# Optimization experiments

Hardware: AMD Instinct MI355X
Metric: run time of the kernel (lower is better)

Reference implementation:

```python
import jax, jax.numpy as jnp
import numpy as np

N_NODES = 50000
N_EDGES = 800000
F_IN, H, C1, C2 = 256, 128, 4, 3


def gcn_conv(x, W, b, src, dst, n_nodes):
    # PyG GCNConv: add self-loops, symmetric normalization D^-1/2 A D^-1/2,
    # linear transform, scatter-add aggregation at dst, then bias.
    loop = jnp.arange(n_nodes, dtype=src.dtype)
    s = jnp.concatenate([src, loop])
    d = jnp.concatenate([dst, loop])
    deg = jax.ops.segment_sum(jnp.ones_like(d, dtype=x.dtype), d, num_segments=n_nodes)
    dinv = jnp.where(deg > 0, jax.lax.rsqrt(deg), 0.0)
    norm = dinv[s] * dinv[d]                      # [E+N]
    h = x @ W                                     # [N, out]
    msg = h[s] * norm[:, None]                    # gather + scale
    out = jax.ops.segment_sum(msg, d, num_segments=n_nodes)  # scatter-add
    return out + b


def setup_inputs() -> dict:
    key = jax.random.key(0)
    ks = jax.random.split(key, 10)
    x = jax.random.normal(ks[0], (N_NODES, F_IN), dtype=jnp.float32)
    edge_index = jax.random.randint(ks[1], (2, N_EDGES), 0, N_NODES, dtype=jnp.int32)
    def lin(k, fan_in, fan_out):
        bound = 1.0 / np.sqrt(fan_in)
        kw, kb = jax.random.split(k)
        W = jax.random.uniform(kw, (fan_in, fan_out), jnp.float32, -bound, bound)
        b = jax.random.uniform(kb, (fan_out,), jnp.float32, -bound, bound)
        return W, b
    W1, b1 = lin(ks[2], F_IN, H)
    W2, b2 = lin(ks[3], H, H)
    Wh1, bh1 = lin(ks[4], H, C1)
    Wh2, bh2 = lin(ks[5], H, C2)
    return {"x": x, "edge_index": edge_index, "W1": W1, "b1": b1,
            "W2": W2, "b2": b2, "Wh1": Wh1, "bh1": bh1, "Wh2": Wh2, "bh2": bh2}


def reference(x, edge_index, W1, b1, W2, b2, Wh1, bh1, Wh2, bh2):
    # Eval-mode forward (dropout p=0.5 is identity at inference; l2_classifier=False).
    src, dst = edge_index[0], edge_index[1]
    h = gcn_conv(x, W1, b1, src, dst, N_NODES)
    h = jax.nn.relu(h)
    h = gcn_conv(h, W2, b2, src, dst, N_NODES)
    out1 = h @ Wh1 + bh1
    out2 = h @ Wh2 + bh2
    return (out1, out2, h)
```

## Files before the change

### kernel.cpp

```cpp
#include <hip/hip_runtime.h>

#define NN 50000
#define NE 800000
#define FIN 256
#define HD 128
#define CAP 96

typedef unsigned int uint;
typedef unsigned short ushort;
typedef __attribute__((ext_vector_type(8))) short short8v;
typedef __attribute__((ext_vector_type(4))) float f32x4;

__device__ inline ushort f2bf(float f) {
    uint u = __float_as_uint(f);
    u += 0x7fffu + ((u >> 16) & 1u);
    return (ushort)(u >> 16);
}
__device__ inline float bf2f(ushort h) { return __uint_as_float(((uint)h) << 16); }
__device__ inline void unpack2(uint u, float& a, float& b) {
    a = __uint_as_float(u << 16);
    b = __uint_as_float(u & 0xffff0000u);
}


__global__ void build_buckets(const int* __restrict__ ei, int* __restrict__ cnt,
                              int* __restrict__ bucket) {
    int e = blockIdx.x * 256 + threadIdx.x;
    if (e >= NE) return;
    int s = ei[e];
    int d = ei[NE + e];
    int pos = atomicAdd(&cnt[d], 1);
    if (pos < CAP) bucket[d * CAP + pos] = s;
}

__global__ void compute_dinv(const int* __restrict__ cnt, float* __restrict__ dinv) {
    int v = blockIdx.x * 256 + threadIdx.x;
    if (v < NN) dinv[v] = rsqrtf((float)cnt[v] + 1.0f);
}


template<int K>
__global__ void prep_wt(const float* __restrict__ W, ushort* __restrict__ Wt) {
    int idx = blockIdx.x * 256 + threadIdx.x;
    if (idx >= K * 128) return;
    int k = idx >> 7, col = idx & 127;
    Wt[col * K + k] = f2bf(W[idx]);
}


template<int K>
__global__ __launch_bounds__(256) void gemm_mfma(const float* __restrict__ A,
                                                 const ushort* __restrict__ Wt,
                                                 const float* __restrict__ dscale,
                                                 ushort* __restrict__ C, int M) {
    __shared__ ushort Ah[64][40];
    __shared__ ushort Al[64][40];
    __shared__ ushort Bt[128][40];
    const int tid  = threadIdx.x;
    const int wid  = tid >> 6;
    const int lane = tid & 63;
    const int fr   = lane & 15;
    const int kg   = lane >> 4;

    const int blockRow = blockIdx.x * 64;

    f32x4 acc[8];
#pragma unroll
    for (int n = 0; n < 8; ++n) acc[n] = (f32x4){0.f, 0.f, 0.f, 0.f};

    const int s_ar = tid >> 3;
    const int s_ak = (tid & 7) << 2;

    for (int k0 = 0; k0 < K; k0 += 32) {
#pragma unroll
        for (int i = 0; i < 2; ++i) {
            int r = i * 32 + s_ar;
            int row = blockRow + r;
            float4 av = make_float4(0.f, 0.f, 0.f, 0.f);
            if (row < M) av = *(const float4*)(A + (size_t)row * K + k0 + s_ak);
            ushort h0 = f2bf(av.x), h1 = f2bf(av.y), h2 = f2bf(av.z), h3 = f2bf(av.w);
            ushort l0 = f2bf(av.x - bf2f(h0)), l1 = f2bf(av.y - bf2f(h1));
            ushort l2 = f2bf(av.z - bf2f(h2)), l3 = f2bf(av.w - bf2f(h3));
            uint2 hw, lw;
            hw.x = (uint)h0 | ((uint)h1 << 16); hw.y = (uint)h2 | ((uint)h3 << 16);
            lw.x = (uint)l0 | ((uint)l1 << 16); lw.y = (uint)l2 | ((uint)l3 << 16);
            *(uint2*)&Ah[r][s_ak] = hw;
            *(uint2*)&Al[r][s_ak] = lw;
        }
#pragma unroll
        for (int i = 0; i < 2; ++i) {
            int id = i * 256 + tid;
            int col = id >> 2;
            int kc = (id & 3) << 3;
            *(uint4*)&Bt[col][kc] = *(const uint4*)(Wt + (size_t)col * K + k0 + kc);
        }
        __syncthreads();
        short8v a_h = *(short8v*)&Ah[(wid << 4) + fr][kg << 3];
        short8v a_l = *(short8v*)&Al[(wid << 4) + fr][kg << 3];
#pragma unroll
        for (int n = 0; n < 8; ++n) {
            short8v b = *(short8v*)&Bt[(n << 4) + fr][kg << 3];
            acc[n] = __builtin_amdgcn_mfma_f32_16x16x32_bf16(a_h, b, acc[n], 0, 0, 0);
            acc[n] = __builtin_amdgcn_mfma_f32_16x16x32_bf16(a_l, b, acc[n], 0, 0, 0);
        }
        __syncthreads();
    }

    const int rbase = blockRow + (wid << 4) + (kg << 2);
#pragma unroll
    for (int r = 0; r < 4; ++r) {
        int row = rbase + r;
        if (row < M) {
            float ds = dscale[row];
#pragma unroll
            for (int n = 0; n < 8; ++n)
                C[(size_t)row * 128 + (n << 4) + fr] = f2bf(ds * acc[n][r]);
        }
    }
}


template<int RELU, int HEADS>
__global__ __launch_bounds__(256) void aggregate(const ushort* __restrict__ hb,
                                                 const int* __restrict__ cnt,
                                                 const int* __restrict__ bucket,
                                                 const float* __restrict__ dinv,
                                                 const float* __restrict__ bias,
                                                 float* __restrict__ out,
                                                 const float* __restrict__ Wh1,
                                                 const float* __restrict__ bh1,
                                                 const float* __restrict__ Wh2,
                                                 const float* __restrict__ bh2,
                                                 float* __restrict__ out1,
                                                 float* __restrict__ out2) {
    int v = (blockIdx.x << 2) + (threadIdx.x >> 6);
    if (v >= NN) return;
    const int lane = threadIdx.x & 63;
    const int g = lane >> 4;
    const int q = lane & 15;
    int c = cnt[v]; if (c > CAP) c = CAP;
    const int total = c + 1;
    const float di = dinv[v];
    const int* bk = bucket + (size_t)v * CAP;

    float acc[8];
#pragma unroll
    for (int j = 0; j < 8; ++j) acc[j] = 0.f;

    auto slotof = [&](int k) -> int {
        return k < c ? bk[k] : (k == c ? v : NN);
    };
    auto rowload = [&](int s) -> uint4 {
        return *(const uint4*)(hb + (size_t)s * 128 + (q << 3));
    };

    int sA = slotof(g);
    int sB = slotof(4 + g);
    uint4 rA = rowload(sA);
    uint4 rB = rowload(sB);
    int sC = slotof(8 + g);
    int sD = slotof(12 + g);

    for (int e = 0; e < total; e += 8) {
        uint4 rA2 = rowload(sC);
        uint4 rB2 = rowload(sD);
        sC = slotof(e + 16 + g);
        sD = slotof(e + 20 + g);
        float f0, f1, f2, f3, f4, f5, f6, f7;
        unpack2(rA.x, f0, f1); unpack2(rA.y, f2, f3);
        unpack2(rA.z, f4, f5); unpack2(rA.w, f6, f7);
        acc[0] += f0; acc[1] += f1; acc[2] += f2; acc[3] += f3;
        acc[4] += f4; acc[5] += f5; acc[6] += f6; acc[7] += f7;
        unpack2(rB.x, f0, f1); unpack2(rB.y, f2, f3);
        unpack2(rB.z, f4, f5); unpack2(rB.w, f6, f7);
        acc[0] += f0; acc[1] += f1; acc[2] += f2; acc[3] += f3;
        acc[4] += f4; acc[5] += f5; acc[6] += f6; acc[7] += f7;
        rA = rA2; rB = rB2;
    }

#pragma unroll
    for (int j = 0; j < 8; ++j) {
        acc[j] += __shfl_xor(acc[j], 16);
        acc[j] += __shfl_xor(acc[j], 32);
    }

    float4 bb0 = *(const float4*)(bias + (q << 3));
    float4 bb1 = *(const float4*)(bias + (q << 3) + 4);
    float o[8];
    o[0] = fmaf(di, acc[0], bb0.x); o[1] = fmaf(di, acc[1], bb0.y);
    o[2] = fmaf(di, acc[2], bb0.z); o[3] = fmaf(di, acc[3], bb0.w);
    o[4] = fmaf(di, acc[4], bb1.x); o[5] = fmaf(di, acc[5], bb1.y);
    o[6] = fmaf(di, acc[6], bb1.z); o[7] = fmaf(di, acc[7], bb1.w);
    if (RELU) {
#pragma unroll
        for (int j = 0; j < 8; ++j) o[j] = fmaxf(o[j], 0.f);
    }

    if (g < 2) {
        int j0 = (g & 1) << 2;
        *(float4*)(out + (size_t)v * 128 + (q << 3) + j0) =
            make_float4(o[j0], o[j0 + 1], o[j0 + 2], o[j0 + 3]);
    }

    if (HEADS) {
        const int kb = q << 3;
        float p[7];
#pragma unroll
        for (int cc = 0; cc < 4; ++cc) {
            float s = 0.f;
#pragma unroll
            for (int j = 0; j < 8; ++j) s = fmaf(o[j], Wh1[(kb + j) * 4 + cc], s);
            p[cc] = s;
        }
#pragma unroll
        for (int cc = 0; cc < 3; ++cc) {
            float s = 0.f;
#pragma unroll
            for (int j = 0; j < 8; ++j) s = fmaf(o[j], Wh2[(kb + j) * 3 + cc], s);
            p[4 + cc] = s;
        }
#pragma unroll
        for (int i = 0; i < 7; ++i) {
            float s = p[i];
            s += __shfl_xor(s, 1);
            s += __shfl_xor(s, 2);
            s += __shfl_xor(s, 4);
            s += __shfl_xor(s, 8);
            p[i] = s;
        }
        if (lane == 0) {
            out1[(size_t)v * 4 + 0] = p[0] + bh1[0];
            out1[(size_t)v * 4 + 1] = p[1] + bh1[1];
            out1[(size_t)v * 4 + 2] = p[2] + bh1[2];
            out1[(size_t)v * 4 + 3] = p[3] + bh1[3];
            out2[(size_t)v * 3 + 0] = p[4] + bh2[0];
            out2[(size_t)v * 3 + 1] = p[5] + bh2[1];
            out2[(size_t)v * 3 + 2] = p[6] + bh2[2];
        }
    }
}


extern "C" void kernel_launch(void* const* d_in, const int* in_sizes, int n_in,
                              void* d_out, int out_size, void* d_ws, size_t ws_size,
                              hipStream_t stream) {
    const float* x   = (const float*)d_in[0];
    const int*   ei  = (const int*)d_in[1];
    const float* W1  = (const float*)d_in[2];
    const float* b1  = (const float*)d_in[3];
    const float* W2  = (const float*)d_in[4];
    const float* b2  = (const float*)d_in[5];
    const float* Wh1 = (const float*)d_in[6];
    const float* bh1 = (const float*)d_in[7];
    const float* Wh2 = (const float*)d_in[8];
    const float* bh2 = (const float*)d_in[9];

    float* out1 = (float*)d_out;
    float* out2 = out1 + (size_t)NN * 4;
    float* hout = out2 + (size_t)NN * 3;

    char* ws = (char*)d_ws;
    auto alloc = [&](size_t bytes) { char* p = ws; ws += (bytes + 255) & ~(size_t)255; return p; };
    int*    cnt    = (int*)   alloc((size_t)NN * 4);
    float*  dinv   = (float*) alloc((size_t)NN * 4);
    int*    bucket = (int*)   alloc((size_t)NN * CAP * 4);
    ushort* hlinb  = (ushort*)alloc((size_t)(NN + 1) * HD * 2);
    float*  hagg   = (float*) alloc((size_t)NN * HD * 4);
    ushort* Wt1    = (ushort*)alloc((size_t)128 * FIN * 2);
    ushort* Wt2    = (ushort*)alloc((size_t)128 * HD * 2);

    hipMemsetAsync(cnt, 0, (size_t)NN * 4, stream);
    hipMemsetAsync(hlinb + (size_t)NN * HD, 0, HD * 2, stream);
    build_buckets<<<(NE + 255) / 256, 256, 0, stream>>>(ei, cnt, bucket);
    compute_dinv<<<(NN + 255) / 256, 256, 0, stream>>>(cnt, dinv);
    prep_wt<FIN><<<(FIN * 128 + 255) / 256, 256, 0, stream>>>(W1, Wt1);
    prep_wt<HD><<<(HD * 128 + 255) / 256, 256, 0, stream>>>(W2, Wt2);

    gemm_mfma<FIN><<<(NN + 63) / 64, 256, 0, stream>>>(x, Wt1, dinv, hlinb, NN);
    aggregate<1, 0><<<(NN + 3) / 4, 256, 0, stream>>>(hlinb, cnt, bucket, dinv, b1, hagg,
                                                      nullptr, nullptr, nullptr, nullptr,
                                                      nullptr, nullptr);

    gemm_mfma<HD><<<(NN + 63) / 64, 256, 0, stream>>>(hagg, Wt2, dinv, hlinb, NN);
    aggregate<0, 1><<<(NN + 3) / 4, 256, 0, stream>>>(hlinb, cnt, bucket, dinv, b2, hout,
                                                      Wh1, bh1, Wh2, bh2, out1, out2);
}
```

Before: 298.2 us.

## Process four nodes per wavefront with a continuous chunk stream in aggregation

```diff
diff --git a/kernel.cpp b/kernel.cpp
--- a/kernel.cpp
+++ b/kernel.cpp
@@ -133,110 +133,130 @@
                                                  const float* __restrict__ bh2,
                                                  float* __restrict__ out1,
                                                  float* __restrict__ out2) {
-    int v = (blockIdx.x << 2) + (threadIdx.x >> 6);
-    if (v >= NN) return;
+    const int wv = blockIdx.x * 4 + (threadIdx.x >> 6);
+    const int v0 = wv << 2;
+    if (v0 >= NN) return;
     const int lane = threadIdx.x & 63;
     const int g = lane >> 4;
     const int q = lane & 15;
-    int c = cnt[v]; if (c > CAP) c = CAP;
-    const int total = c + 1;
-    const float di = dinv[v];
-    const int* bk = bucket + (size_t)v * CAP;
-
-    float acc[8];
-#pragma unroll
-    for (int j = 0; j < 8; ++j) acc[j] = 0.f;
-
-    auto slotof = [&](int k) -> int {
-        return k < c ? bk[k] : (k == c ? v : NN);
+
+    const int c0 = min(cnt[v0], CAP),     c1 = min(cnt[v0 + 1], CAP),
+              c2 = min(cnt[v0 + 2], CAP), c3 = min(cnt[v0 + 3], CAP);
+    const float di0 = dinv[v0],     di1 = dinv[v0 + 1],
+                di2 = dinv[v0 + 2], di3 = dinv[v0 + 3];
+    const int tb1 = (c0 + 4) >> 2;
+    const int tb2 = tb1 + ((c1 + 4) >> 2);
+    const int tb3 = tb2 + ((c2 + 4) >> 2);
+    const int nch = tb3 + ((c3 + 4) >> 2);
+
+    auto slot_index = [&](int t) -> int {
+        if (t >= nch) return NN;
+        int nd = (t >= tb1) + (t >= tb2) + (t >= tb3);
+        int tb = nd == 0 ? 0  : nd == 1 ? tb1 : nd == 2 ? tb2 : tb3;
+        int c  = nd == 0 ? c0 : nd == 1 ? c1  : nd == 2 ? c2  : c3;
+        int idx = ((t - tb) << 2) + g;
+        int vv = v0 + nd;
+        return idx < c ? bucket[(size_t)vv * CAP + idx] : (idx == c ? vv : NN);
     };
     auto rowload = [&](int s) -> uint4 {
         return *(const uint4*)(hb + (size_t)s * 128 + (q << 3));
     };
 
-    int sA = slotof(g);
-    int sB = slotof(4 + g);
-    uint4 rA = rowload(sA);
-    uint4 rB = rowload(sB);
-    int sC = slotof(8 + g);
-    int sD = slotof(12 + g);
-
-    for (int e = 0; e < total; e += 8) {
-        uint4 rA2 = rowload(sC);
-        uint4 rB2 = rowload(sD);
-        sC = slotof(e + 16 + g);
-        sD = slotof(e + 20 + g);
+    float acc[8];
+#pragma unroll
+    for (int j = 0; j < 8; ++j) acc[j] = 0.f;
+
+    auto consume = [&](uint4 r) {
         float f0, f1, f2, f3, f4, f5, f6, f7;
-        unpack2(rA.x, f0, f1); unpack2(rA.y, f2, f3);
-        unpack2(rA.z, f4, f5); unpack2(rA.w, f6, f7);
+        unpack2(r.x, f0, f1); unpack2(r.y, f2, f3);
+        unpack2(r.z, f4, f5); unpack2(r.w, f6, f7);
         acc[0] += f0; acc[1] += f1; acc[2] += f2; acc[3] += f3;
         acc[4] += f4; acc[5] += f5; acc[6] += f6; acc[7] += f7;
-        unpack2(rB.x, f0, f1); unpack2(rB.y, f2, f3);
-        unpack2(rB.z, f4, f5); unpack2(rB.w, f6, f7);
-        acc[0] += f0; acc[1] += f1; acc[2] += f2; acc[3] += f3;
-        acc[4] += f4; acc[5] += f5; acc[6] += f6; acc[7] += f7;
-        rA = rA2; rB = rB2;
-    }
-
-#pragma unroll
-    for (int j = 0; j < 8; ++j) {
-        acc[j] += __shfl_xor(acc[j], 16);
-        acc[j] += __shfl_xor(acc[j], 32);
-    }
-
-    float4 bb0 = *(const float4*)(bias + (q << 3));
-    float4 bb1 = *(const float4*)(bias + (q << 3) + 4);
-    float o[8];
-    o[0] = fmaf(di, acc[0], bb0.x); o[1] = fmaf(di, acc[1], bb0.y);
-    o[2] = fmaf(di, acc[2], bb0.z); o[3] = fmaf(di, acc[3], bb0.w);
-    o[4] = fmaf(di, acc[4], bb1.x); o[5] = fmaf(di, acc[5], bb1.y);
-    o[6] = fmaf(di, acc[6], bb1.z); o[7] = fmaf(di, acc[7], bb1.w);
-    if (RELU) {
-#pragma unroll
-        for (int j = 0; j < 8; ++j) o[j] = fmaxf(o[j], 0.f);
-    }
-
-    if (g < 2) {
-        int j0 = (g & 1) << 2;
-        *(float4*)(out + (size_t)v * 128 + (q << 3) + j0) =
-            make_float4(o[j0], o[j0 + 1], o[j0 + 2], o[j0 + 3]);
-    }
-
-    if (HEADS) {
-        const int kb = q << 3;
-        float p[7];
-#pragma unroll
-        for (int cc = 0; cc < 4; ++cc) {
-            float s = 0.f;
-#pragma unroll
-            for (int j = 0; j < 8; ++j) s = fmaf(o[j], Wh1[(kb + j) * 4 + cc], s);
-            p[cc] = s;
-        }
-#pragma unroll
-        for (int cc = 0; cc < 3; ++cc) {
-            float s = 0.f;
-#pragma unroll
-            for (int j = 0; j < 8; ++j) s = fmaf(o[j], Wh2[(kb + j) * 3 + cc], s);
-            p[4 + cc] = s;
-        }
-#pragma unroll
-        for (int i = 0; i < 7; ++i) {
-            float s = p[i];
-            s += __shfl_xor(s, 1);
-            s += __shfl_xor(s, 2);
-            s += __shfl_xor(s, 4);
-            s += __shfl_xor(s, 8);
-            p[i] = s;
-        }
-        if (lane == 0) {
-            out1[(size_t)v * 4 + 0] = p[0] + bh1[0];
-            out1[(size_t)v * 4 + 1] = p[1] + bh1[1];
-            out1[(size_t)v * 4 + 2] = p[2] + bh1[2];
-            out1[(size_t)v * 4 + 3] = p[3] + bh1[3];
-            out2[(size_t)v * 3 + 0] = p[4] + bh2[0];
-            out2[(size_t)v * 3 + 1] = p[5] + bh2[1];
-            out2[(size_t)v * 3 + 2] = p[6] + bh2[2];
-        }
+    };
+
+    auto flush = [&](int nd) {
+        float o[8];
+#pragma unroll
+        for (int j = 0; j < 8; ++j) {
+            float t = acc[j];
+            t += __shfl_xor(t, 16);
+            t += __shfl_xor(t, 32);
+            o[j] = t;
+            acc[j] = 0.f;
+        }
+        const float di = nd == 0 ? di0 : nd == 1 ? di1 : nd == 2 ? di2 : di3;
+        const int v = v0 + nd;
+        float4 bb0 = *(const float4*)(bias + (q << 3));
+        float4 bb1 = *(const float4*)(bias + (q << 3) + 4);
+        o[0] = fmaf(di, o[0], bb0.x); o[1] = fmaf(di, o[1], bb0.y);
+        o[2] = fmaf(di, o[2], bb0.z); o[3] = fmaf(di, o[3], bb0.w);
+        o[4] = fmaf(di, o[4], bb1.x); o[5] = fmaf(di, o[5], bb1.y);
+        o[6] = fmaf(di, o[6], bb1.z); o[7] = fmaf(di, o[7], bb1.w);
+        if (RELU) {
+#pragma unroll
+            for (int j = 0; j < 8; ++j) o[j] = fmaxf(o[j], 0.f);
+        }
+        if (g < 2) {
+            int j0 = (g & 1) << 2;
+            *(float4*)(out + (size_t)v * 128 + (q << 3) + j0) =
+                make_float4(o[j0], o[j0 + 1], o[j0 + 2], o[j0 + 3]);
+        }
+        if (HEADS) {
+            const int kb = q << 3;
+            float p[7];
+#pragma unroll
+            for (int cc = 0; cc < 4; ++cc) {
+                float s = 0.f;
+#pragma unroll
+                for (int j = 0; j < 8; ++j) s = fmaf(o[j], Wh1[(kb + j) * 4 + cc], s);
+                p[cc] = s;
+            }
+#pragma unroll
+            for (int cc = 0; cc < 3; ++cc) {
+                float s = 0.f;
+#pragma unroll
+                for (int j = 0; j < 8; ++j) s = fmaf(o[j], Wh2[(kb + j) * 3 + cc], s);
+                p[4 + cc] = s;
+            }
+#pragma unroll
+            for (int i = 0; i < 7; ++i) {
+                float s = p[i];
+                s += __shfl_xor(s, 1);
+                s += __shfl_xor(s, 2);
+                s += __shfl_xor(s, 4);
+                s += __shfl_xor(s, 8);
+                p[i] = s;
+            }
+            if (lane == 0) {
+                out1[(size_t)v * 4 + 0] = p[0] + bh1[0];
+                out1[(size_t)v * 4 + 1] = p[1] + bh1[1];
+                out1[(size_t)v * 4 + 2] = p[2] + bh1[2];
+                out1[(size_t)v * 4 + 3] = p[3] + bh1[3];
+                out2[(size_t)v * 3 + 0] = p[4] + bh2[0];
+                out2[(size_t)v * 3 + 1] = p[5] + bh2[1];
+                out2[(size_t)v * 3 + 2] = p[6] + bh2[2];
+            }
+        }
+    };
+
+    int sP2 = slot_index(2);
+    int sP3 = slot_index(3);
+    uint4 rA = rowload(slot_index(0));
+    uint4 rB = rowload(slot_index(1));
+
+    int nd = 0;
+    int flushT = tb1 - 1;
+    for (int t = 0; t < nch; ++t) {
+        uint4 rN = rowload(sP2);
+        sP2 = sP3;
+        sP3 = slot_index(t + 4);
+        consume(rA);
+        if (t == flushT) {
+            flush(nd);
+            ++nd;
+            flushT = nd == 1 ? tb2 - 1 : nd == 2 ? tb3 - 1 : nch - 1;
+        }
+        rA = rB; rB = rN;
     }
 }
 
@@ -277,11 +297,11 @@
     prep_wt<HD><<<(HD * 128 + 255) / 256, 256, 0, stream>>>(W2, Wt2);
 
     gemm_mfma<FIN><<<(NN + 63) / 64, 256, 0, stream>>>(x, Wt1, dinv, hlinb, NN);
-    aggregate<1, 0><<<(NN + 3) / 4, 256, 0, stream>>>(hlinb, cnt, bucket, dinv, b1, hagg,
-                                                      nullptr, nullptr, nullptr, nullptr,
-                                                      nullptr, nullptr);
+    aggregate<1, 0><<<(NN + 15) / 16, 256, 0, stream>>>(hlinb, cnt, bucket, dinv, b1, hagg,
+                                                        nullptr, nullptr, nullptr, nullptr,
+                                                        nullptr, nullptr);
 
     gemm_mfma<HD><<<(NN + 63) / 64, 256, 0, stream>>>(hagg, Wt2, dinv, hlinb, NN);
-    aggregate<0, 1><<<(NN + 3) / 4, 256, 0, stream>>>(hlinb, cnt, bucket, dinv, b2, hout,
-                                                      Wh1, bh1, Wh2, bh2, out1, out2);
-}
+    aggregate<0, 1><<<(NN + 15) / 16, 256, 0, stream>>>(hlinb, cnt, bucket, dinv, b2, hout,
+                                                        Wh1, bh1, Wh2, bh2, out1, out2);
+}
```

Measured after the change: 411.3 us. 1.38x slower.
